# Optimization experiments

Hardware: AMD Instinct MI355X
Metric: run time of the kernel (lower is better)

The kernel has to match this reference:

```python
import jax, jax.numpy as jnp
import numpy as np

EPS = 1e-5

def _bn_relu(y, mean, var, scale, bias):
    # y: (b, c, n); eval-mode batchnorm over channel axis, then ReLU
    inv = scale / jnp.sqrt(var + EPS)
    return jax.nn.relu((y - mean[None, :, None]) * inv[None, :, None] + bias[None, :, None])

def setup_inputs() -> dict:
    key = jax.random.key(0)
    ks = jax.random.split(key, 6)
    b, c, n, cr = 4, 256, 4096, 32
    inp = {
        'x': jax.random.normal(ks[0], (b, c, n), jnp.float32),
        'w_q': jax.random.normal(ks[1], (cr, c), jnp.float32) * (1.0 / np.sqrt(c)),
        'w_k': jax.random.normal(ks[2], (cr, c), jnp.float32) * (1.0 / np.sqrt(c)),
        'w_v': jax.random.normal(ks[3], (c, c), jnp.float32) * (1.0 / np.sqrt(c)),
        'bn1_scale': jnp.ones((cr,), jnp.float32), 'bn1_bias': jnp.zeros((cr,), jnp.float32),
        'bn1_mean': jnp.zeros((cr,), jnp.float32), 'bn1_var': jnp.ones((cr,), jnp.float32),
        'bn2_scale': jnp.ones((cr,), jnp.float32), 'bn2_bias': jnp.zeros((cr,), jnp.float32),
        'bn2_mean': jnp.zeros((cr,), jnp.float32), 'bn2_var': jnp.ones((cr,), jnp.float32),
        'bn3_scale': jnp.ones((c,), jnp.float32), 'bn3_bias': jnp.zeros((c,), jnp.float32),
        'bn3_mean': jnp.zeros((c,), jnp.float32), 'bn3_var': jnp.ones((c,), jnp.float32),
        'gamma': jax.random.normal(ks[4], (1,), jnp.float32),
    }
    return inp

def reference(x, w_q, w_k, w_v,
              bn1_scale, bn1_bias, bn1_mean, bn1_var,
              bn2_scale, bn2_bias, bn2_mean, bn2_var,
              bn3_scale, bn3_bias, bn3_mean, bn3_var,
              gamma):
    # x: (b, c, n). Original views as (b, c, n, 1) so width=1, height=n.
    b, c, n = x.shape
    # 1x1 conv == channel matmul, then BN+ReLU
    q = _bn_relu(jnp.einsum('oc,bcn->bon', w_q, x), bn1_mean, bn1_var, bn1_scale, bn1_bias)  # (b, c', n)
    k = _bn_relu(jnp.einsum('oc,bcn->bon', w_k, x), bn2_mean, bn2_var, bn2_scale, bn2_bias)  # (b, c', n)
    v = _bn_relu(jnp.einsum('oc,bcn->bon', w_v, x), bn3_mean, bn3_var, bn3_scale, bn3_bias)  # (b, c, n)
    # energy_H: (b, n, n) with -inf diagonal (self-attention along 'height')
    energy_h = jnp.einsum('bdi,bdj->bij', q, k)
    eye = jnp.eye(n, dtype=bool)
    energy_h = jnp.where(eye[None], -jnp.inf, energy_h)
    # energy_W: width=1 -> per-position self energy (b, n)
    energy_w = jnp.sum(q * k, axis=1)
    # softmax over concat of n H-logits and 1 W-logit
    att = jax.nn.softmax(jnp.concatenate([energy_h, energy_w[..., None]], axis=-1), axis=-1)  # (b, n, n+1)
    att_h = att[..., :n]        # (b, n, n), query i -> key j
    att_w = att[..., n]         # (b, n)
    out_h = jnp.einsum('bcj,bij->bci', v, att_h)   # aggregate values along height
    out_w = v * att_w[:, None, :]                  # width=1 self term
    out = gamma[0] * (out_h + out_w) + x
    return out
```

## Files before the change

### kernel.cpp

```cpp
#include <hip/hip_runtime.h>

#define Bb 4
#define Cc 256
#define Nn 4096
#define CR 32
#define EPS_BN 1e-5f
#define SHIFT2 28.853900817779268f
#define LOG2E  1.4426950408889634f
#define JSPLIT 4
#define JSL (Nn / JSPLIT)
#define TJ 64
#define NTILES (JSL / TJ)

typedef __attribute__((ext_vector_type(8))) short short8;
typedef __attribute__((ext_vector_type(4))) float f32x4;

__device__ inline unsigned int pk2(float a, float b) {
    __bf16 ha = (__bf16)a, hb = (__bf16)b;
    unsigned short ra = __builtin_bit_cast(unsigned short, ha);
    unsigned short rb = __builtin_bit_cast(unsigned short, hb);
    return ((unsigned int)rb << 16) | ra;
}
__device__ inline float blo(unsigned int u) { return __uint_as_float(u << 16); }
__device__ inline float bhi(unsigned int u) { return __uint_as_float(u & 0xffff0000u); }
__device__ inline float ex2(float x) { return __builtin_amdgcn_exp2f(x); }

__global__ __launch_bounds__(256) void qkv_kernel(
    const float* __restrict__ x,
    const float* __restrict__ wq, const float* __restrict__ wk, const float* __restrict__ wv,
    const float* __restrict__ bn1s, const float* __restrict__ bn1b, const float* __restrict__ bn1m, const float* __restrict__ bn1v,
    const float* __restrict__ bn2s, const float* __restrict__ bn2b, const float* __restrict__ bn2m, const float* __restrict__ bn2v,
    const float* __restrict__ bn3s, const float* __restrict__ bn3b, const float* __restrict__ bn3m, const float* __restrict__ bn3v,
    __bf16* __restrict__ Qt, __bf16* __restrict__ Kt, __bf16* __restrict__ Vb)
{
    __shared__ __align__(16) __bf16 F[16384];
    __shared__ __align__(16) float  sXf[4][32 * 40];
    __shared__ __align__(16) __bf16 sXt[4][2][32 * 40];

    const int tid = threadIdx.x;
    const int n0 = blockIdx.x * 128, g = blockIdx.y, b = blockIdx.z;
    const int lane = tid & 63, w = tid >> 6;
    const int l15 = lane & 15, l4 = lane >> 4;

    {
        int r = tid >> 2, q = tid & 3;
        int R = g * 64 + r;
        const float* src = (R < 32) ? (wq + (size_t)R * Cc)
                         : (R < 64) ? (wk + (size_t)(R - 32) * Cc)
                                    : (wv + (size_t)(R - 64) * Cc);
        int mt = r >> 4, l15r = r & 15;
#pragma unroll
        for (int u8 = 0; u8 < 8; ++u8) {
            float4 a = *(const float4*)&src[q * 64 + u8 * 8];
            float4 c2 = *(const float4*)&src[q * 64 + u8 * 8 + 4];
            uint4 p = { pk2(a.x,a.y), pk2(a.z,a.w), pk2(c2.x,c2.y), pk2(c2.z,c2.w) };
            int kc = 2 * q + (u8 >> 2), l4k = u8 & 3;
            *(uint4*)&F[(((kc * 4 + mt) * 64 + l4k * 16 + l15r)) * 8] = p;
        }
    }

    float*  sXfw  = &sXf[w][0];
    __bf16* sXtw0 = &sXt[w][0][0];
    __bf16* sXtw1 = &sXt[w][1][0];

    const int cr = lane >> 3, nq = lane & 7;
    const float* xbase = x + (size_t)(b * Cc + cr) * Nn + n0 + w * 32 + nq * 4;

    float4 xg[4];
#pragma unroll
    for (int it = 0; it < 4; ++it)
        xg[it] = *(const float4*)&xbase[(size_t)(it * 8) * Nn];

    __syncthreads();

    f32x4 acc[4][2];
#pragma unroll
    for (int mt = 0; mt < 4; ++mt)
#pragma unroll
        for (int nt = 0; nt < 2; ++nt) acc[mt][nt] = (f32x4){0.f, 0.f, 0.f, 0.f};

    for (int kc = 0; kc < 8; ++kc) {
#pragma unroll
        for (int it = 0; it < 4; ++it)
            *(float4*)&sXfw[(it * 8 + cr) * 40 + nq * 4] = xg[it];

        if (kc + 1 < 8) {
#pragma unroll
            for (int it = 0; it < 4; ++it)
                xg[it] = *(const float4*)&xbase[(size_t)((kc + 1) * 32 + it * 8) * Nn];
        }

#pragma unroll
        for (int s = 0; s < 2; ++s) {
            int n = lane & 31, c0 = (lane >> 5) * 8 + s * 16;
            float h[8], lo[8];
#pragma unroll
            for (int j = 0; j < 8; ++j) {
                float v = sXfw[(c0 + j) * 40 + n];
                float hh = (float)(__bf16)v;
                h[j] = hh; lo[j] = v - hh;
            }
            uint4 H = { pk2(h[0],h[1]), pk2(h[2],h[3]), pk2(h[4],h[5]), pk2(h[6],h[7]) };
            uint4 L = { pk2(lo[0],lo[1]), pk2(lo[2],lo[3]), pk2(lo[4],lo[5]), pk2(lo[6],lo[7]) };
            *(uint4*)&sXtw0[n * 40 + c0] = H;
            *(uint4*)&sXtw1[n * 40 + c0] = L;
        }

        short8 bh[2], bl[2];
#pragma unroll
        for (int nt = 0; nt < 2; ++nt) {
            bh[nt] = *(const short8*)&sXtw0[(nt * 16 + l15) * 40 + l4 * 8];
            bl[nt] = *(const short8*)&sXtw1[(nt * 16 + l15) * 40 + l4 * 8];
        }
#pragma unroll
        for (int mt = 0; mt < 4; ++mt) {
            short8 af = *(const short8*)&F[((kc * 4 + mt) * 64 + lane) * 8];
#pragma unroll
            for (int nt = 0; nt < 2; ++nt) {
                acc[mt][nt] = __builtin_amdgcn_mfma_f32_16x16x32_bf16(af, bh[nt], acc[mt][nt], 0, 0, 0);
                acc[mt][nt] = __builtin_amdgcn_mfma_f32_16x16x32_bf16(af, bl[nt], acc[mt][nt], 0, 0, 0);
            }
        }
    }

    if (g == 0) {
#pragma unroll
        for (int mt = 0; mt < 4; ++mt) {
            float scl[4], off[4];
#pragma unroll
            for (int r = 0; r < 4; ++r) {
                int R = mt * 16 + l4 * 4 + r;
                float s, o;
                if (R < 32) {
                    s = bn1s[R] * __frsqrt_rn(bn1v[R] + EPS_BN);
                    o = bn1b[R] - bn1m[R] * s;
                } else {
                    int row = R - 32;
                    s = bn2s[row] * __frsqrt_rn(bn2v[row] + EPS_BN);
                    o = bn2b[row] - bn2m[row] * s;
                    s *= LOG2E; o *= LOG2E;
                }
                scl[r] = s; off[r] = o;
            }
            __bf16* dst = (mt < 2) ? Qt : Kt;
            int d0 = (mt & 1) * 16 + l4 * 4;
#pragma unroll
            for (int nt = 0; nt < 2; ++nt) {
                f32x4 a = acc[mt][nt];
                float e0 = fmaxf(fmaf(a.x, scl[0], off[0]), 0.f);
                float e1 = fmaxf(fmaf(a.y, scl[1], off[1]), 0.f);
                float e2 = fmaxf(fmaf(a.z, scl[2], off[2]), 0.f);
                float e3 = fmaxf(fmaf(a.w, scl[3], off[3]), 0.f);
                uint2 p = { pk2(e0, e1), pk2(e2, e3) };
                int n = n0 + w * 32 + nt * 16 + l15;
                *(uint2*)&dst[(size_t)(b * Nn + n) * CR + d0] = p;
            }
        }
    } else {
        __bf16* oT = F;
        __syncthreads();
#pragma unroll
        for (int mt = 0; mt < 4; ++mt) {
            float scl[4], off[4];
#pragma unroll
            for (int r = 0; r < 4; ++r) {
                int row = (g - 1) * 64 + mt * 16 + l4 * 4 + r;
                float s = bn3s[row] * __frsqrt_rn(bn3v[row] + EPS_BN);
                scl[r] = s; off[r] = bn3b[row] - bn3m[row] * s;
            }
#pragma unroll
            for (int nt = 0; nt < 2; ++nt) {
                f32x4 a = acc[mt][nt];
                float e[4];
                e[0] = fmaxf(fmaf(a.x, scl[0], off[0]), 0.f);
                e[1] = fmaxf(fmaf(a.y, scl[1], off[1]), 0.f);
                e[2] = fmaxf(fmaf(a.z, scl[2], off[2]), 0.f);
                e[3] = fmaxf(fmaf(a.w, scl[3], off[3]), 0.f);
                int ncol = w * 32 + nt * 16 + l15;
#pragma unroll
                for (int r = 0; r < 4; ++r)
                    oT[(mt * 16 + l4 * 4 + r) * 136 + ncol] = (__bf16)e[r];
            }
        }
        __syncthreads();
        int rr = tid >> 2, qq = tid & 3;
        size_t vrow = (size_t)(b * Cc + (g - 1) * 64 + rr) * Nn + n0 + qq * 32;
#pragma unroll
        for (int e8 = 0; e8 < 4; ++e8)
            *(uint4*)&Vb[vrow + e8 * 8] = *(const uint4*)&oT[rr * 136 + qq * 32 + e8 * 8];
    }
}

__global__ __launch_bounds__(256) void attn_kernel(
    const __bf16* __restrict__ Qt, const __bf16* __restrict__ Kt,
    const __bf16* __restrict__ Vb,
    __bf16* __restrict__ PO, float* __restrict__ PL)
{
    __shared__ __align__(16) __bf16 sQ[64 * 40];
    __shared__ __align__(16) __bf16 sP[2][64 * 72];
    __shared__ __align__(16) float  sL[4][64];

    const int tid = threadIdx.x, lane = tid & 63, w = tid >> 6;
    const int b = blockIdx.z, js = blockIdx.y, iblk = blockIdx.x;
    const int i0 = iblk * 64;
    const int l15 = lane & 15, l4 = lane >> 4;

    {
        int i = tid >> 2, o = tid & 3;
        *(uint4*)&sQ[i * 40 + o * 8] =
            *(const uint4*)&Qt[(size_t)(b * Nn + i0 + i) * CR + o * 8];
    }
    __syncthreads();
    short8 qf[4];
#pragma unroll
    for (int it = 0; it < 4; ++it)
        qf[it] = *(const short8*)&sQ[(it * 16 + l15) * 40 + l4 * 8];

    f32x4 oacc[16];
#pragma unroll
    for (int z = 0; z < 16; ++z) oacc[z] = (f32x4){0.f, 0.f, 0.f, 0.f};
    float lp[4] = {0.f, 0.f, 0.f, 0.f};

    const size_t jb = (size_t)js * JSL;
    short8 kf = *(const short8*)&Kt[(size_t)(b * Nn + jb + 16 * w + l15) * CR + l4 * 8];
    short8 vf[8];
#pragma unroll
    for (int u = 0; u < 8; ++u) {
        int jh = u >> 2, ct = u & 3;
        int c = w * 64 + ct * 16 + l15;
        vf[u] = *(const short8*)&Vb[(size_t)(b * Cc + c) * Nn + jb + (jh * 4 + l4) * 8];
    }

    for (int t = 0; t < NTILES; ++t) {
        const size_t j0 = jb + (size_t)t * TJ;
        __bf16* sPb = sP[t & 1];

#pragma unroll
        for (int it = 0; it < 4; ++it) {
            f32x4 c0 = (f32x4){0.f, 0.f, 0.f, 0.f};
            c0 = __builtin_amdgcn_mfma_f32_16x16x32_bf16(kf, qf[it], c0, 0, 0, 0);
            float e0 = ex2(c0.x - SHIFT2);
            float e1 = ex2(c0.y - SHIFT2);
            float e2 = ex2(c0.z - SHIFT2);
            float e3 = ex2(c0.w - SHIFT2);
            lp[it] += (e0 + e1) + (e2 + e3);
            uint2 p2 = { pk2(e0, e1), pk2(e2, e3) };
            *(uint2*)&sPb[(it * 16 + l15) * 72 + w * 16 + l4 * 4] = p2;
        }
        __syncthreads();

        if (t + 1 < NTILES)
            kf = *(const short8*)&Kt[(size_t)(b * Nn + j0 + TJ + 16 * w + l15) * CR + l4 * 8];

#pragma unroll
        for (int jh = 0; jh < 2; ++jh) {
            short8 pf[4];
#pragma unroll
            for (int it = 0; it < 4; ++it)
                pf[it] = *(const short8*)&sPb[(it * 16 + l15) * 72 + jh * 32 + l4 * 8];
#pragma unroll
            for (int ct = 0; ct < 4; ++ct) {
#pragma unroll
                for (int it = 0; it < 4; ++it)
                    oacc[it * 4 + ct] = __builtin_amdgcn_mfma_f32_16x16x32_bf16(
                        pf[it], vf[jh * 4 + ct], oacc[it * 4 + ct], 0, 0, 0);
            }
        }

        if (t + 1 < NTILES) {
#pragma unroll
            for (int u = 0; u < 8; ++u) {
                int jh = u >> 2, ct = u & 3;
                int c = w * 64 + ct * 16 + l15;
                vf[u] = *(const short8*)&Vb[(size_t)(b * Cc + c) * Nn + j0 + TJ + (jh * 4 + l4) * 8];
            }
        }
    }

#pragma unroll
    for (int it = 0; it < 4; ++it) {
        float v = lp[it];
        v += __shfl_xor(v, 16);
        v += __shfl_xor(v, 32);
        if (lane < 16) sL[w][it * 16 + lane] = v;
    }
    __syncthreads();
    if (tid < 64)
        PL[(size_t)(js * Bb + b) * Nn + i0 + tid] =
            sL[0][tid] + sL[1][tid] + sL[2][tid] + sL[3][tid];

    const size_t base = (size_t)((js * Bb + b) * (Nn / 64) + iblk) * 16384;
#pragma unroll
    for (int it = 0; it < 4; ++it)
#pragma unroll
        for (int ct = 0; ct < 4; ++ct) {
            f32x4 a = oacc[it * 4 + ct];
            uint2 p = { pk2(a.x, a.y), pk2(a.z, a.w) };
            *(uint2*)&PO[base + (size_t)((((w * 4 + it) * 4 + ct) * 64 + lane)) * 4] = p;
        }
}

__global__ __launch_bounds__(256) void reduce_kernel(
    const __bf16* __restrict__ PO, const float* __restrict__ PL,
    const float* __restrict__ x, const float* __restrict__ gamma,
    float* __restrict__ out)
{
    __shared__ __align__(16) float oT[64 * 68];
    __shared__ float sLinv[64];

    const int tid = threadIdx.x;
    const int iblk = blockIdx.x, wq = blockIdx.y, b = blockIdx.z;
    const int i0 = iblk * 64;
    const int lane = tid & 63, ct = tid >> 6, l15 = lane & 15, l4 = lane >> 4;

    if (tid < 64) {
        float l = 0.f;
#pragma unroll
        for (int js = 0; js < JSPLIT; ++js)
            l += PL[(size_t)(js * Bb + b) * Nn + i0 + tid];
        sLinv[tid] = 1.0f / l;
    }

    float o[4][4];
#pragma unroll
    for (int it = 0; it < 4; ++it) {
        o[it][0] = o[it][1] = o[it][2] = o[it][3] = 0.f;
#pragma unroll
        for (int js = 0; js < JSPLIT; ++js) {
            size_t base = (size_t)((js * Bb + b) * (Nn / 64) + iblk) * 16384;
            uint2 v = *(const uint2*)&PO[base + (size_t)((((wq * 4 + it) * 4 + ct) * 64 + lane)) * 4];
            o[it][0] += blo(v.x); o[it][1] += bhi(v.x);
            o[it][2] += blo(v.y); o[it][3] += bhi(v.y);
        }
    }

    const int cl = ct * 16 + l15;
#pragma unroll
    for (int it = 0; it < 4; ++it) {
        float4 t4 = { o[it][0], o[it][1], o[it][2], o[it][3] };
        *(float4*)&oT[cl * 68 + it * 16 + l4 * 4] = t4;
    }
    __syncthreads();

    const float g = gamma[0];
    const int c_l = tid >> 2, icol = (tid & 3) * 16;
    const int cg = wq * 64 + c_l;
    const size_t gb = (size_t)(b * Cc + cg) * Nn + i0 + icol;
#pragma unroll
    for (int k4 = 0; k4 < 4; ++k4) {
        float4 ov = *(const float4*)&oT[c_l * 68 + icol + k4 * 4];
        float4 li = *(const float4*)&sLinv[icol + k4 * 4];
        float4 xv = *(const float4*)&x[gb + k4 * 4];
        float4 res;
        res.x = fmaf(g, ov.x * li.x, xv.x);
        res.y = fmaf(g, ov.y * li.y, xv.y);
        res.z = fmaf(g, ov.z * li.z, xv.z);
        res.w = fmaf(g, ov.w * li.w, xv.w);
        *(float4*)&out[gb + k4 * 4] = res;
    }
}

extern "C" void kernel_launch(void* const* d_in, const int* in_sizes, int n_in,
                              void* d_out, int out_size, void* d_ws, size_t ws_size,
                              hipStream_t stream)
{
    const float* x    = (const float*)d_in[0];
    const float* wq   = (const float*)d_in[1];
    const float* wk   = (const float*)d_in[2];
    const float* wv   = (const float*)d_in[3];
    const float* bn1s = (const float*)d_in[4];
    const float* bn1b = (const float*)d_in[5];
    const float* bn1m = (const float*)d_in[6];
    const float* bn1v = (const float*)d_in[7];
    const float* bn2s = (const float*)d_in[8];
    const float* bn2b = (const float*)d_in[9];
    const float* bn2m = (const float*)d_in[10];
    const float* bn2v = (const float*)d_in[11];
    const float* bn3s = (const float*)d_in[12];
    const float* bn3b = (const float*)d_in[13];
    const float* bn3m = (const float*)d_in[14];
    const float* bn3v = (const float*)d_in[15];
    const float* gmm  = (const float*)d_in[16];
    float* out = (float*)d_out;

    char* ws = (char*)d_ws;
    __bf16* Qt  = (__bf16*)(ws);
    __bf16* Kt  = (__bf16*)(ws + (1u << 20));
    __bf16* Vb  = (__bf16*)(ws + (2u << 20));
    char*   big = ws + (10u << 20);
    __bf16* PO  = (__bf16*)big;
    float*  PL  = (float*)(big + 33554432);

    qkv_kernel<<<dim3(Nn / 128, 5, Bb), 256, 0, stream>>>(
        x, wq, wk, wv,
        bn1s, bn1b, bn1m, bn1v,
        bn2s, bn2b, bn2m, bn2v,
        bn3s, bn3b, bn3m, bn3v,
        Qt, Kt, Vb);

    attn_kernel<<<dim3(Nn / 64, JSPLIT, Bb), 256, 0, stream>>>(Qt, Kt, Vb, PO, PL);

    reduce_kernel<<<dim3(Nn / 64, 4, Bb), 256, 0, stream>>>(PO, PL, x, gmm, out);
}
```

Before: 213.4 us.

## Drop key split and fuse reduction epilogue into attention kernel

```diff
diff --git a/kernel.cpp b/kernel.cpp
--- a/kernel.cpp
+++ b/kernel.cpp
@@ -7,10 +7,8 @@
 #define EPS_BN 1e-5f
 #define SHIFT2 28.853900817779268f
 #define LOG2E  1.4426950408889634f
-#define JSPLIT 4
-#define JSL (Nn / JSPLIT)
 #define TJ 64
-#define NTILES (JSL / TJ)
+#define NT (Nn / TJ)
 
 typedef __attribute__((ext_vector_type(8))) short short8;
 typedef __attribute__((ext_vector_type(4))) float f32x4;
@@ -21,8 +19,6 @@
     unsigned short rb = __builtin_bit_cast(unsigned short, hb);
     return ((unsigned int)rb << 16) | ra;
 }
-__device__ inline float blo(unsigned int u) { return __uint_as_float(u << 16); }
-__device__ inline float bhi(unsigned int u) { return __uint_as_float(u & 0xffff0000u); }
 __device__ inline float ex2(float x) { return __builtin_amdgcn_exp2f(x); }
 
 __global__ __launch_bounds__(256) void qkv_kernel(
@@ -193,50 +189,56 @@
 
 __global__ __launch_bounds__(256) void attn_kernel(
     const __bf16* __restrict__ Qt, const __bf16* __restrict__ Kt,
-    const __bf16* __restrict__ Vb,
-    __bf16* __restrict__ PO, float* __restrict__ PL)
+    const __bf16* __restrict__ Vb, const float* __restrict__ x,
+    const float* __restrict__ gamma, float* __restrict__ out)
 {
-    __shared__ __align__(16) __bf16 sQ[64 * 40];
-    __shared__ __align__(16) __bf16 sP[2][64 * 72];
-    __shared__ __align__(16) float  sL[4][64];
+    __shared__ __align__(16) char U[36864];
+    __bf16* sQ  = (__bf16*)U;
+    __bf16* sP0 = (__bf16*)(U + 2560);
+    __bf16* sP1 = (__bf16*)(U + 2560 + 4608);
+    float*  oT  = (float*)U;
+    __shared__ float sL[4][32];
+    __shared__ float sLinv[32];
 
     const int tid = threadIdx.x, lane = tid & 63, w = tid >> 6;
-    const int b = blockIdx.z, js = blockIdx.y, iblk = blockIdx.x;
-    const int i0 = iblk * 64;
+    const int id = blockIdx.x;
+    const int xcd = id & 7;
+    const int b = xcd >> 1;
+    const int iblk = (xcd & 1) * 64 + (id >> 3);
+    const int i0 = iblk * 32;
     const int l15 = lane & 15, l4 = lane >> 4;
 
-    {
+    if (tid < 128) {
         int i = tid >> 2, o = tid & 3;
         *(uint4*)&sQ[i * 40 + o * 8] =
             *(const uint4*)&Qt[(size_t)(b * Nn + i0 + i) * CR + o * 8];
     }
     __syncthreads();
-    short8 qf[4];
-#pragma unroll
-    for (int it = 0; it < 4; ++it)
+    short8 qf[2];
+#pragma unroll
+    for (int it = 0; it < 2; ++it)
         qf[it] = *(const short8*)&sQ[(it * 16 + l15) * 40 + l4 * 8];
 
-    f32x4 oacc[16];
-#pragma unroll
-    for (int z = 0; z < 16; ++z) oacc[z] = (f32x4){0.f, 0.f, 0.f, 0.f};
-    float lp[4] = {0.f, 0.f, 0.f, 0.f};
-
-    const size_t jb = (size_t)js * JSL;
-    short8 kf = *(const short8*)&Kt[(size_t)(b * Nn + jb + 16 * w + l15) * CR + l4 * 8];
+    f32x4 oacc[8];
+#pragma unroll
+    for (int z = 0; z < 8; ++z) oacc[z] = (f32x4){0.f, 0.f, 0.f, 0.f};
+    float lp[2] = {0.f, 0.f};
+
+    short8 kf = *(const short8*)&Kt[(size_t)(b * Nn + 16 * w + l15) * CR + l4 * 8];
     short8 vf[8];
 #pragma unroll
     for (int u = 0; u < 8; ++u) {
         int jh = u >> 2, ct = u & 3;
         int c = w * 64 + ct * 16 + l15;
-        vf[u] = *(const short8*)&Vb[(size_t)(b * Cc + c) * Nn + jb + (jh * 4 + l4) * 8];
-    }
-
-    for (int t = 0; t < NTILES; ++t) {
-        const size_t j0 = jb + (size_t)t * TJ;
-        __bf16* sPb = sP[t & 1];
-
-#pragma unroll
-        for (int it = 0; it < 4; ++it) {
+        vf[u] = *(const short8*)&Vb[(size_t)(b * Cc + c) * Nn + (jh * 4 + l4) * 8];
+    }
+
+    for (int t = 0; t < NT; ++t) {
+        const size_t j0 = (size_t)t * TJ;
+        __bf16* sPb = (t & 1) ? sP1 : sP0;
+
+#pragma unroll
+        for (int it = 0; it < 2; ++it) {
             f32x4 c0 = (f32x4){0.f, 0.f, 0.f, 0.f};
             c0 = __builtin_amdgcn_mfma_f32_16x16x32_bf16(kf, qf[it], c0, 0, 0, 0);
             float e0 = ex2(c0.x - SHIFT2);
@@ -249,25 +251,25 @@
         }
         __syncthreads();
 
-        if (t + 1 < NTILES)
+        if (t + 1 < NT)
             kf = *(const short8*)&Kt[(size_t)(b * Nn + j0 + TJ + 16 * w + l15) * CR + l4 * 8];
 
 #pragma unroll
         for (int jh = 0; jh < 2; ++jh) {
-            short8 pf[4];
-#pragma unroll
-            for (int it = 0; it < 4; ++it)
+            short8 pf[2];
+#pragma unroll
+            for (int it = 0; it < 2; ++it)
                 pf[it] = *(const short8*)&sPb[(it * 16 + l15) * 72 + jh * 32 + l4 * 8];
 #pragma unroll
             for (int ct = 0; ct < 4; ++ct) {
 #pragma unroll
-                for (int it = 0; it < 4; ++it)
+                for (int it = 0; it < 2; ++it)
                     oacc[it * 4 + ct] = __builtin_amdgcn_mfma_f32_16x16x32_bf16(
                         pf[it], vf[jh * 4 + ct], oacc[it * 4 + ct], 0, 0, 0);
             }
         }
 
-        if (t + 1 < NTILES) {
+        if (t + 1 < NT) {
 #pragma unroll
             for (int u = 0; u < 8; ++u) {
                 int jh = u >> 2, ct = u & 3;
@@ -278,85 +280,46 @@
     }
 
 #pragma unroll
-    for (int it = 0; it < 4; ++it) {
+    for (int it = 0; it < 2; ++it) {
         float v = lp[it];
         v += __shfl_xor(v, 16);
         v += __shfl_xor(v, 32);
         if (lane < 16) sL[w][it * 16 + lane] = v;
     }
     __syncthreads();
-    if (tid < 64)
-        PL[(size_t)(js * Bb + b) * Nn + i0 + tid] =
-            sL[0][tid] + sL[1][tid] + sL[2][tid] + sL[3][tid];
-
-    const size_t base = (size_t)((js * Bb + b) * (Nn / 64) + iblk) * 16384;
-#pragma unroll
-    for (int it = 0; it < 4; ++it)
+    if (tid < 32)
+        sLinv[tid] = 1.0f / (sL[0][tid] + sL[1][tid] + sL[2][tid] + sL[3][tid]);
+
+#pragma unroll
+    for (int it = 0; it < 2; ++it)
 #pragma unroll
         for (int ct = 0; ct < 4; ++ct) {
             f32x4 a = oacc[it * 4 + ct];
-            uint2 p = { pk2(a.x, a.y), pk2(a.z, a.w) };
-            *(uint2*)&PO[base + (size_t)((((w * 4 + it) * 4 + ct) * 64 + lane)) * 4] = p;
-        }
-}
-
-__global__ __launch_bounds__(256) void reduce_kernel(
-    const __bf16* __restrict__ PO, const float* __restrict__ PL,
-    const float* __restrict__ x, const float* __restrict__ gamma,
-    float* __restrict__ out)
-{
-    __shared__ __align__(16) float oT[64 * 68];
-    __shared__ float sLinv[64];
-
-    const int tid = threadIdx.x;
-    const int iblk = blockIdx.x, wq = blockIdx.y, b = blockIdx.z;
-    const int i0 = iblk * 64;
-    const int lane = tid & 63, ct = tid >> 6, l15 = lane & 15, l4 = lane >> 4;
-
-    if (tid < 64) {
-        float l = 0.f;
-#pragma unroll
-        for (int js = 0; js < JSPLIT; ++js)
-            l += PL[(size_t)(js * Bb + b) * Nn + i0 + tid];
-        sLinv[tid] = 1.0f / l;
-    }
-
-    float o[4][4];
-#pragma unroll
-    for (int it = 0; it < 4; ++it) {
-        o[it][0] = o[it][1] = o[it][2] = o[it][3] = 0.f;
-#pragma unroll
-        for (int js = 0; js < JSPLIT; ++js) {
-            size_t base = (size_t)((js * Bb + b) * (Nn / 64) + iblk) * 16384;
-            uint2 v = *(const uint2*)&PO[base + (size_t)((((wq * 4 + it) * 4 + ct) * 64 + lane)) * 4];
-            o[it][0] += blo(v.x); o[it][1] += bhi(v.x);
-            o[it][2] += blo(v.y); o[it][3] += bhi(v.y);
-        }
-    }
-
-    const int cl = ct * 16 + l15;
-#pragma unroll
-    for (int it = 0; it < 4; ++it) {
-        float4 t4 = { o[it][0], o[it][1], o[it][2], o[it][3] };
-        *(float4*)&oT[cl * 68 + it * 16 + l4 * 4] = t4;
-    }
+            int c = w * 64 + ct * 16 + l15;
+            int i = it * 16 + l4 * 4;
+            float4 t4 = { a.x, a.y, a.z, a.w };
+            *(float4*)&oT[c * 36 + i] = t4;
+        }
+    const float g = gamma[0];
     __syncthreads();
 
-    const float g = gamma[0];
-    const int c_l = tid >> 2, icol = (tid & 3) * 16;
-    const int cg = wq * 64 + c_l;
-    const size_t gb = (size_t)(b * Cc + cg) * Nn + i0 + icol;
-#pragma unroll
-    for (int k4 = 0; k4 < 4; ++k4) {
-        float4 ov = *(const float4*)&oT[c_l * 68 + icol + k4 * 4];
-        float4 li = *(const float4*)&sLinv[icol + k4 * 4];
-        float4 xv = *(const float4*)&x[gb + k4 * 4];
-        float4 res;
-        res.x = fmaf(g, ov.x * li.x, xv.x);
-        res.y = fmaf(g, ov.y * li.y, xv.y);
-        res.z = fmaf(g, ov.z * li.z, xv.z);
-        res.w = fmaf(g, ov.w * li.w, xv.w);
-        *(float4*)&out[gb + k4 * 4] = res;
+#pragma unroll
+    for (int half = 0; half < 2; ++half) {
+        int c_l = tid >> 1, icol = (tid & 1) * 16;
+        int cg = half * 128 + c_l;
+        size_t gb = (size_t)(b * Cc + cg) * Nn + i0 + icol;
+#pragma unroll
+        for (int k4 = 0; k4 < 4; ++k4) {
+            float4 ov = *(const float4*)&oT[cg * 36 + icol + k4 * 4];
+            float4 li = *(const float4*)&sLinv[icol + k4 * 4];
+            float4 xv = *(const float4*)&x[gb + k4 * 4];
+            float4 res;
+            res.x = fmaf(g, ov.x * li.x, xv.x);
+            res.y = fmaf(g, ov.y * li.y, xv.y);
+            res.z = fmaf(g, ov.z * li.z, xv.z);
+            res.w = fmaf(g, ov.w * li.w, xv.w);
+            *(float4*)&out[gb + k4 * 4] = res;
+        }
     }
 }
 
@@ -387,9 +350,6 @@
     __bf16* Qt  = (__bf16*)(ws);
     __bf16* Kt  = (__bf16*)(ws + (1u << 20));
     __bf16* Vb  = (__bf16*)(ws + (2u << 20));
-    char*   big = ws + (10u << 20);
-    __bf16* PO  = (__bf16*)big;
-    float*  PL  = (float*)(big + 33554432);
 
     qkv_kernel<<<dim3(Nn / 128, 5, Bb), 256, 0, stream>>>(
         x, wq, wk, wv,
@@ -398,7 +358,5 @@
         bn3s, bn3b, bn3m, bn3v,
         Qt, Kt, Vb);
 
-    attn_kernel<<<dim3(Nn / 64, JSPLIT, Bb), 256, 0, stream>>>(Qt, Kt, Vb, PO, PL);
-
-    reduce_kernel<<<dim3(Nn / 64, 4, Bb), 256, 0, stream>>>(PO, PL, x, gmm, out);
+    attn_kernel<<<dim3(Bb * (Nn / 32)), 256, 0, stream>>>(Qt, Kt, Vb, x, gmm, out);
 }
```

Result: slower. 263.1 us (+23.3%).
